# Kernel tuning notes

Hardware: AMD Instinct MI355X
Metric: run time of the kernel (lower is better)

Reference implementation:

```python
import jax, jax.numpy as jnp
import numpy as np

KERNEL_SIZE = 5


def setup_inputs() -> dict:
    key = jax.random.key(0)
    k1, k2 = jax.random.split(key)
    x = jax.random.normal(k1, (4, 32, 256, 256), dtype=jnp.float32)
    kernel = jax.random.normal(k2, (4, KERNEL_SIZE * KERNEL_SIZE, 256, 256), dtype=jnp.float32)
    return {"x": x, "kernel": kernel}


def reference(x, kernel):
    k = KERNEL_SIZE
    b, kk, h, w = kernel.shape
    # softmax over the k*k dim (original permutes to channels-last then softmax dim=-1)
    kern = jax.nn.softmax(jnp.transpose(kernel, (0, 2, 3, 1)), axis=-1)  # [b,h,w,k*k]
    pad = (k - 1) // 2
    # replicate padding on spatial dims
    xp = jnp.pad(x, ((0, 0), (0, 0), (pad, pad), (pad, pad)), mode="edge")
    # unfold: patch index order is di*k + dj (height offset first), matching torch unfold(2).unfold(3)
    patches = jnp.stack(
        [xp[:, :, i:i + h, j:j + w] for i in range(k) for j in range(k)], axis=-1
    )  # [b,c,h,w,k*k]
    # per-pixel softmax-weighted local sum; kernel broadcast over channel dim
    out = jnp.sum(patches * kern[:, None, :, :, :], axis=-1)  # [b,c,h,w]
    return out
```

## Files before the change

### kernel.cpp

```cpp
#include <hip/hip_runtime.h>

#define HW    256
#define HW2   (HW*HW)
#define KTAPS 25
#define TW    32
#define TH    8
#define LW    36
#define LH    12
#define NEL   (LW*LH)
#define NSTG  7
#define CPB   8
#define C     32

__device__ __forceinline__ void stage_issue(float r[NSTG], const float* __restrict__ xc,
                                            int lane, int h0, int w0) {
#pragma unroll
    for (int k = 0; k < NSTG; ++k) {
        int idx = lane + k * 64;
        if (idx < NEL) {
            int i  = idx / LW;
            int j  = idx - i * LW;
            int hh = min(max(h0 + i - 2, 0), HW - 1);
            int ww = min(max(w0 + j - 2, 0), HW - 1);
            r[k] = xc[hh * HW + ww];
        }
    }
}

__global__ __launch_bounds__(64, 3) void ddown_kernel(
    const float* __restrict__ x,
    const float* __restrict__ kern,
    float* __restrict__ out)
{
    __shared__ __align__(16) float xt[NEL];

    const int lane = threadIdx.x;
    const int txq  = lane & 7;
    const int ty   = lane >> 3;
    const int w0   = blockIdx.x * TW;
    const int h0   = blockIdx.y * TH;
    const int b    = blockIdx.z >> 2;
    const int c0   = (blockIdx.z & 3) * CPB;

    const int h = h0 + ty;
    const int w = w0 + txq * 4;

    const float* xb = x + (size_t)(b * C + c0) * HW2;

    float r[NSTG];
    stage_issue(r, xb, lane, h0, w0);

    const float* kb = kern + (size_t)b * KTAPS * HW2 + h * HW + w;
    float4 wt[KTAPS];
    float sx = 0.f, sy = 0.f, sz = 0.f, sw = 0.f;
#pragma unroll
    for (int j = 0; j < KTAPS; ++j) {
        float4 v = *(const float4*)(kb + (size_t)j * HW2);
        v.x = __expf(v.x); v.y = __expf(v.y); v.z = __expf(v.z); v.w = __expf(v.w);
        sx += v.x; sy += v.y; sz += v.z; sw += v.w;
        wt[j] = v;
    }
    const float ix = 1.f / sx, iy = 1.f / sy, iz = 1.f / sz, iw = 1.f / sw;

    float* ob = out + (size_t)(b * C + c0) * HW2 + h * HW + w;

    for (int cc = 0; cc < CPB; ++cc) {
#pragma unroll
        for (int k = 0; k < NSTG; ++k) {
            int idx = lane + k * 64;
            if (idx < NEL) xt[idx] = r[k];
        }
        if (cc + 1 < CPB) stage_issue(r, xb + (size_t)(cc + 1) * HW2, lane, h0, w0);

        float ax = 0.f, ay = 0.f, az = 0.f, aw = 0.f;
#pragma unroll
        for (int di = 0; di < 5; ++di) {
            const float* row = &xt[(ty + di) * LW + txq * 4];
            float4 pa = *(const float4*)(row);
            float4 pb = *(const float4*)(row + 4);
            float w8[8] = {pa.x, pa.y, pa.z, pa.w, pb.x, pb.y, pb.z, pb.w};
#pragma unroll
            for (int dj = 0; dj < 5; ++dj) {
                float4 wv = wt[di * 5 + dj];
                ax += wv.x * w8[dj + 0];
                ay += wv.y * w8[dj + 1];
                az += wv.z * w8[dj + 2];
                aw += wv.w * w8[dj + 3];
            }
        }
        float4 res = { ax * ix, ay * iy, az * iz, aw * iw };
        *(float4*)(ob + (size_t)cc * HW2) = res;
    }
}

extern "C" void kernel_launch(void* const* d_in, const int* in_sizes, int n_in,
                              void* d_out, int out_size, void* d_ws, size_t ws_size,
                              hipStream_t stream) {
    const float* x    = (const float*)d_in[0];
    const float* kern = (const float*)d_in[1];
    float* out        = (float*)d_out;

    dim3 grid(HW / TW, HW / TH, 4 * 4);
    ddown_kernel<<<grid, 64, 0, stream>>>(x, kern, out);
}
```

Before: 110.5 us.

## Replace LDS tile staging with direct float2 global loads and larger blocks

Drops the shared-memory halo tile and its register prefetch pipeline. Each thread now reads its 5x4 float2 neighbourhood straight from global memory, relying on L1/L2 cache for reuse, and fixes the replicate padding at the edges with per-lane select flags. Blocks grow from 64 to 128 threads (16 rows), which halves the grid. This removes LDS writes and reads and the staging overhead, but it raises redundant global and cache traffic and loses the explicit prefetch overlap across channels.

```diff
diff --git a/kernel.cpp b/kernel.cpp
--- a/kernel.cpp
+++ b/kernel.cpp
@@ -2,59 +2,30 @@
 
 #define HW    256
 #define HW2   (HW*HW)
-#define KTAPS 25
-#define TW    32
-#define TH    8
-#define LW    36
-#define LH    12
-#define NEL   (LW*LH)
-#define NSTG  7
+#define C     32
 #define CPB   8
-#define C     32
 
-__device__ __forceinline__ void stage_issue(float r[NSTG], const float* __restrict__ xc,
-                                            int lane, int h0, int w0) {
-#pragma unroll
-    for (int k = 0; k < NSTG; ++k) {
-        int idx = lane + k * 64;
-        if (idx < NEL) {
-            int i  = idx / LW;
-            int j  = idx - i * LW;
-            int hh = min(max(h0 + i - 2, 0), HW - 1);
-            int ww = min(max(w0 + j - 2, 0), HW - 1);
-            r[k] = xc[hh * HW + ww];
-        }
-    }
-}
-
-__global__ __launch_bounds__(64, 3) void ddown_kernel(
+__global__ __launch_bounds__(128, 2) void ddown_kernel(
     const float* __restrict__ x,
     const float* __restrict__ kern,
     float* __restrict__ out)
 {
-    __shared__ __align__(16) float xt[NEL];
-
-    const int lane = threadIdx.x;
-    const int txq  = lane & 7;
-    const int ty   = lane >> 3;
-    const int w0   = blockIdx.x * TW;
-    const int h0   = blockIdx.y * TH;
-    const int b    = blockIdx.z >> 2;
-    const int c0   = (blockIdx.z & 3) * CPB;
+    const int t   = threadIdx.x;
+    const int txq = t & 7;
+    const int ty  = t >> 3;
+    const int w0  = blockIdx.x * 32;
+    const int h0  = blockIdx.y * 16;
+    const int b   = blockIdx.z >> 2;
+    const int c0  = (blockIdx.z & 3) * CPB;
 
     const int h = h0 + ty;
-    const int w = w0 + txq * 4;
+    const int c = w0 + txq * 4;
 
-    const float* xb = x + (size_t)(b * C + c0) * HW2;
-
-    float r[NSTG];
-    stage_issue(r, xb, lane, h0, w0);
-
-    const float* kb = kern + (size_t)b * KTAPS * HW2 + h * HW + w;
-    float4 wt[KTAPS];
+    const float* kb = kern + (size_t)b * 25 * HW2 + h * HW + c;
+    float4 wt[25];
     float sx = 0.f, sy = 0.f, sz = 0.f, sw = 0.f;
 #pragma unroll
-    for (int j = 0; j < KTAPS; ++j) {
+    for (int j = 0; j < 25; ++j) {
         float4 v = *(const float4*)(kb + (size_t)j * HW2);
         v.x = __expf(v.x); v.y = __expf(v.y); v.z = __expf(v.z); v.w = __expf(v.w);
         sx += v.x; sy += v.y; sz += v.z; sw += v.w;
@@ -62,23 +33,41 @@
     }
     const float ix = 1.f / sx, iy = 1.f / sy, iz = 1.f / sz, iw = 1.f / sw;
 
-    float* ob = out + (size_t)(b * C + c0) * HW2 + h * HW + w;
+    int row_off[5];
+#pragma unroll
+    for (int di = 0; di < 5; ++di) {
+        int hr = h - 2 + di;
+        hr = min(max(hr, 0), HW - 1);
+        row_off[di] = hr * HW;
+    }
+    int colp[4];
+#pragma unroll
+    for (int k = 0; k < 4; ++k) {
+        int p = (c - 2 + 2 * k) / 2;
+        p = min(max(p, 0), HW / 2 - 1);
+        colp[k] = p * 2;
+    }
+    const bool lfix = (c == 0);
+    const bool rfix = (c == HW - 4);
+
+    const float* xc = x + (size_t)(b * C + c0) * HW2;
+    float*       ob = out + (size_t)(b * C + c0) * HW2 + h * HW + c;
 
     for (int cc = 0; cc < CPB; ++cc) {
+        float2 p[5][4];
 #pragma unroll
-        for (int k = 0; k < NSTG; ++k) {
-            int idx = lane + k * 64;
-            if (idx < NEL) xt[idx] = r[k];
-        }
-        if (cc + 1 < CPB) stage_issue(r, xb + (size_t)(cc + 1) * HW2, lane, h0, w0);
+        for (int di = 0; di < 5; ++di)
+#pragma unroll
+            for (int k = 0; k < 4; ++k)
+                p[di][k] = *(const float2*)(xc + row_off[di] + colp[k]);
 
         float ax = 0.f, ay = 0.f, az = 0.f, aw = 0.f;
 #pragma unroll
         for (int di = 0; di < 5; ++di) {
-            const float* row = &xt[(ty + di) * LW + txq * 4];
-            float4 pa = *(const float4*)(row);
-            float4 pb = *(const float4*)(row + 4);
-            float w8[8] = {pa.x, pa.y, pa.z, pa.w, pb.x, pb.y, pb.z, pb.w};
+            float w8[8] = { p[di][0].x, p[di][0].y, p[di][1].x, p[di][1].y,
+                            p[di][2].x, p[di][2].y, p[di][3].x, p[di][3].y };
+            w8[1] = lfix ? w8[0] : w8[1];
+            w8[6] = rfix ? w8[5] : w8[6];
 #pragma unroll
             for (int dj = 0; dj < 5; ++dj) {
                 float4 wv = wt[di * 5 + dj];
@@ -89,7 +78,9 @@
             }
         }
         float4 res = { ax * ix, ay * iy, az * iz, aw * iw };
-        *(float4*)(ob + (size_t)cc * HW2) = res;
+        *(float4*)ob = res;
+        xc += HW2;
+        ob += HW2;
     }
 }
 
@@ -100,6 +91,6 @@
     const float* kern = (const float*)d_in[1];
     float* out        = (float*)d_out;
 
-    dim3 grid(HW / TW, HW / TH, 4 * 4);
-    ddown_kernel<<<grid, 64, 0, stream>>>(x, kern, out);
+    dim3 grid(HW / 32, HW / 16, 4 * 4);
+    ddown_kernel<<<grid, 128, 0, stream>>>(x, kern, out);
 }
```

Result: slower. 179.0 us (+62.0%).
